# Kernel optimization log

Hardware: AMD Instinct MI355X
Metric: run time of the kernel (lower is better)

## Reference

```python
import jax, jax.numpy as jnp
import numpy as np

V, D, H, L, FF, T, B, W = 32000, 1024, 16, 8, 4096, 1024, 2, 256
HALF = FF // 2
HD = D // H
EPS = 1e-5


def layer_norm(x, g, b):
    mu = jnp.mean(x, axis=-1, keepdims=True)
    var = jnp.mean(jnp.square(x - mu), axis=-1, keepdims=True)
    return (x - mu) * jax.lax.rsqrt(var + EPS) * g + b


def setup_inputs() -> dict:
    key = jax.random.key(0)
    ks = jax.random.split(key, 12)
    s = 0.02
    nrm = lambda k, shape: jax.random.normal(k, shape, jnp.float32) * s
    idx = jax.random.randint(ks[0], (B, T), 0, V, dtype=jnp.int64)
    return {
        "idx": idx,
        "tok_emb": nrm(ks[1], (V, D)),
        "pos_emb": nrm(ks[2], (T, D)),
        "ln1_g": jnp.ones((L, D), jnp.float32),
        "ln1_b": jnp.zeros((L, D), jnp.float32),
        "qkv_w": nrm(ks[3], (L, 3 * D, D)),
        "out_w": nrm(ks[4], (L, D, D)),
        "ln2_g": jnp.ones((L, D), jnp.float32),
        "ln2_b": jnp.zeros((L, D), jnp.float32),
        "a_w1": nrm(ks[5], (L, HALF, D)),
        "a_w2": nrm(ks[6], (L, D, HALF)),
        "f_w1": nrm(ks[7], (L, HALF, D)),
        "f_w2": nrm(ks[8], (L, D, HALF)),
        "lnf_g": jnp.ones((D,), jnp.float32),
        "lnf_b": jnp.zeros((D,), jnp.float32),
        "head_w": nrm(ks[9], (V, D)),
    }


def _forward(idx, tok_emb, pos_emb, ln1_g, ln1_b, qkv_w, out_w, ln2_g, ln2_b,
             a_w1, a_w2, f_w1, f_w2, lnf_g, lnf_b, head_w):
    Bc, Tc = idx.shape
    x = tok_emb[idx] + pos_emb[:Tc]  # [B,T,D]
    # sliding-window causal band: attend to j in [i-W+1, i]
    i = jnp.arange(Tc)
    d = i[:, None] - i[None, :]
    mask = jnp.where((d >= 0) & (d < W), 0.0, -jnp.inf).astype(x.dtype)  # [T,T]
    scale = 1.0 / np.sqrt(HD)

    def block(x, p):
        l1g, l1b, qw, ow, l2g, l2b, aw1, aw2, fw1, fw2 = p
        h = layer_norm(x, l1g, l1b)
        qkv = (h @ qw.T).reshape(Bc, Tc, 3, H, HD)
        q, k, v = qkv[:, :, 0], qkv[:, :, 1], qkv[:, :, 2]  # [B,T,H,HD]
        attn = jnp.einsum('bqhd,bkhd->bhqk', q, k) * scale + mask
        attn = jax.nn.softmax(attn, axis=-1)
        o = jnp.einsum('bhqk,bkhd->bqhd', attn, v).reshape(Bc, Tc, D)
        x = x + o @ ow.T
        h2 = layer_norm(x, l2g, l2b)
        mlp = (jax.nn.gelu(h2 @ aw1.T, approximate=False) @ aw2.T
               + jax.nn.gelu(h2 @ fw1.T, approximate=False) @ fw2.T)
        return x + mlp, None

    x, _ = jax.lax.scan(block, x, (ln1_g, ln1_b, qkv_w, out_w, ln2_g, ln2_b,
                                   a_w1, a_w2, f_w1, f_w2))
    return layer_norm(x, lnf_g, lnf_b) @ head_w.T  # [B,T,V]


def reference(idx, tok_emb, pos_emb, ln1_g, ln1_b, qkv_w, out_w, ln2_g, ln2_b,
              a_w1, a_w2, f_w1, f_w2, lnf_g, lnf_b, head_w):
    return _forward(idx, tok_emb, pos_emb, ln1_g, ln1_b, qkv_w, out_w,
                    ln2_g, ln2_b, a_w1, a_w2, f_w1, f_w2, lnf_g, lnf_b, head_w)
```

## Files before the change

kernel.cpp:

```cpp
#include <hip/hip_runtime.h>

typedef __bf16 bf16x8 __attribute__((ext_vector_type(8)));
typedef __bf16 bf16x4 __attribute__((ext_vector_type(4)));
typedef float  f32x4  __attribute__((ext_vector_type(4)));
typedef unsigned int u32x4 __attribute__((ext_vector_type(4)));

#define MFMA16(a, b, c) __builtin_amdgcn_mfma_f32_16x16x32_bf16(a, b, c, 0, 0, 0)

__device__ __forceinline__ void gload_lds16(const void* g, void* l) {
  __builtin_amdgcn_global_load_lds(
      (const __attribute__((address_space(1))) void*)g,
      (__attribute__((address_space(3))) void*)l, 16, 0, 0);
}

__device__ __forceinline__ void waitvm(int vm) {
  if (vm == 6)      asm volatile("s_waitcnt vmcnt(6)" ::: "memory");
  else if (vm == 4) asm volatile("s_waitcnt vmcnt(4)" ::: "memory");
  else if (vm == 3) asm volatile("s_waitcnt vmcnt(3)" ::: "memory");
  else              asm volatile("s_waitcnt vmcnt(0)" ::: "memory");
}

__global__ __launch_bounds__(256) void cvt_kernel(
    const float* __restrict__ s, __bf16* __restrict__ d, int n8) {
  int i = blockIdx.x * 256 + threadIdx.x;
  if (i >= n8) return;
  size_t o = (size_t)i * 8;
  f32x4 a = *(const f32x4*)(s + o), b = *(const f32x4*)(s + o + 4);
  bf16x8 v;
  v[0] = (__bf16)a[0]; v[1] = (__bf16)a[1]; v[2] = (__bf16)a[2]; v[3] = (__bf16)a[3];
  v[4] = (__bf16)b[0]; v[5] = (__bf16)b[1]; v[6] = (__bf16)b[2]; v[7] = (__bf16)b[3];
  *(bf16x8*)(d + o) = v;
}

__global__ __launch_bounds__(256) void cat_w1_kernel(
    const float* __restrict__ a, const float* __restrict__ f, __bf16* __restrict__ d) {
  int i = blockIdx.x * 256 + threadIdx.x;
  int k = (i & 127) * 8;
  int r = i >> 7;
  const float* s = (r < 2048) ? a + ((size_t)r << 10) + k
                              : f + ((size_t)(r - 2048) << 10) + k;
  f32x4 va = *(const f32x4*)s, vb = *(const f32x4*)(s + 4);
  bf16x8 v;
  v[0] = (__bf16)va[0]; v[1] = (__bf16)va[1]; v[2] = (__bf16)va[2]; v[3] = (__bf16)va[3];
  v[4] = (__bf16)vb[0]; v[5] = (__bf16)vb[1]; v[6] = (__bf16)vb[2]; v[7] = (__bf16)vb[3];
  *(bf16x8*)(d + ((size_t)i << 3)) = v;
}

__global__ __launch_bounds__(256) void cat_w2_kernel(
    const float* __restrict__ a, const float* __restrict__ f, __bf16* __restrict__ d) {
  int i = blockIdx.x * 256 + threadIdx.x;
  int k = (i & 511) * 8;
  int r = i >> 9;
  const float* s = (k < 2048) ? a + (size_t)r * 2048 + k
                              : f + (size_t)r * 2048 + (k - 2048);
  f32x4 va = *(const f32x4*)s, vb = *(const f32x4*)(s + 4);
  bf16x8 v;
  v[0] = (__bf16)va[0]; v[1] = (__bf16)va[1]; v[2] = (__bf16)va[2]; v[3] = (__bf16)va[3];
  v[4] = (__bf16)vb[0]; v[5] = (__bf16)vb[1]; v[6] = (__bf16)vb[2]; v[7] = (__bf16)vb[3];
  *(bf16x8*)(d + ((size_t)i << 3)) = v;
}

__global__ __launch_bounds__(256) void embed_kernel(
    const int* __restrict__ idx, const float* __restrict__ te,
    const float* __restrict__ pe, float* __restrict__ x) {
  int m = blockIdx.x;
  int t = m & 1023;
  int tok = idx[m];
  int c = threadIdx.x * 4;
  f32x4 a = *(const f32x4*)(te + (size_t)tok * 1024 + c);
  f32x4 p = *(const f32x4*)(pe + (size_t)t * 1024 + c);
  *(f32x4*)(x + (size_t)m * 1024 + c) = a + p;
}

__global__ __launch_bounds__(256) void ln_kernel(
    const float* __restrict__ x, const float* __restrict__ g,
    const float* __restrict__ bb, __bf16* __restrict__ out) {
  int row = blockIdx.x, tid = threadIdx.x;
  int wid = tid >> 6, lane = tid & 63;
  f32x4 v = *(const f32x4*)(x + (size_t)row * 1024 + tid * 4);
  float s = v[0] + v[1] + v[2] + v[3];
  #pragma unroll
  for (int off = 32; off >= 1; off >>= 1) s += __shfl_xor(s, off);
  __shared__ float red1[4], red2[4];
  if (lane == 0) red1[wid] = s;
  __syncthreads();
  float mu = (red1[0] + red1[1] + red1[2] + red1[3]) * (1.0f / 1024.0f);
  float d0 = v[0] - mu, d1 = v[1] - mu, d2 = v[2] - mu, d3 = v[3] - mu;
  float q = d0 * d0 + d1 * d1 + d2 * d2 + d3 * d3;
  #pragma unroll
  for (int off = 32; off >= 1; off >>= 1) q += __shfl_xor(q, off);
  if (lane == 0) red2[wid] = q;
  __syncthreads();
  float var = (red2[0] + red2[1] + red2[2] + red2[3]) * (1.0f / 1024.0f);
  float inv = rsqrtf(var + 1e-5f);
  f32x4 gg = *(const f32x4*)(g + tid * 4);
  f32x4 bv = *(const f32x4*)(bb + tid * 4);
  bf16x4 o4;
  o4[0] = (__bf16)(d0 * inv * gg[0] + bv[0]);
  o4[1] = (__bf16)(d1 * inv * gg[1] + bv[1]);
  o4[2] = (__bf16)(d2 * inv * gg[2] + bv[2]);
  o4[3] = (__bf16)(d3 * inv * gg[3] + bv[3]);
  *(bf16x4*)(out + (size_t)row * 1024 + tid * 4) = o4;
}

template <int EPI>
__global__ __launch_bounds__(512, 2) void gemm256(
    const __bf16* __restrict__ A, int lda,
    const __bf16* __restrict__ B, int ldb, int K,
    float* __restrict__ Cf, __bf16* __restrict__ Cb, int ldc, int nbx) {
  __shared__ __align__(16) __bf16 lds[49152];
  const int tid = threadIdx.x, lane = tid & 63, w = tid >> 6;
  const int l15 = lane & 15, l4 = lane >> 4;
  const int wr = w >> 2, wc = w & 3;

  int nwg = gridDim.x, id = blockIdx.x;
  int q = nwg >> 3, r = nwg & 7;
  int xcd = id & 7, pos = id >> 3;
  int nid = (xcd < r ? xcd * (q + 1) : r * (q + 1) + (xcd - r) * q) + pos;
  int row0 = (nid % nbx) * 256, col0 = (nid / nbx) * 256;

  const __bf16* ag = A + (size_t)row0 * lda;
  const __bf16* bg = B + (size_t)col0 * ldb;

  f32x4 acc[8][4];
  #pragma unroll
  for (int i = 0; i < 8; ++i)
    #pragma unroll
    for (int j = 0; j < 4; ++j) acc[i][j] = (f32x4){0.f, 0.f, 0.f, 0.f};

  int srow[2], scol[2];
  #pragma unroll
  for (int i = 0; i < 2; ++i) {
    int p = (w + i * 8) * 1024 + lane * 16;
    int row = p >> 6, ch = (p >> 4) & 3;
    srow[i] = row;
    scol[i] = (ch ^ ((row >> 1) & 3)) * 8;
  }
  const int fx = (((l4 << 4) ^ (((l15 >> 1) & 3) << 4)) >> 1);

  auto stageA = [&](int t, int c) {
    #pragma unroll
    for (int i = 0; i < 2; ++i)
      gload_lds16(ag + (size_t)srow[i] * lda + t * 32 + scol[i],
                  &lds[c * 16384 + (w + i * 8) * 512]);
  };
  auto stageB = [&](int t, int c) {
    #pragma unroll
    for (int i = 0; i < 2; ++i)
      gload_lds16(bg + (size_t)srow[i] * ldb + t * 32 + scol[i],
                  &lds[c * 16384 + 8192 + (w + i * 8) * 512]);
  };

  auto kgroup = [&](int t2, int c, int cn, int vm, bool stg) {
    if (stg) stageA(t2, cn);
    waitvm(vm);
    __builtin_amdgcn_sched_barrier(0);
    __builtin_amdgcn_s_barrier();
    __builtin_amdgcn_sched_barrier(0);
    const int cb = c * 16384;
    bf16x8 bfr[4], af[4];
    #pragma unroll
    for (int ni = 0; ni < 4; ++ni)
      bfr[ni] = *(const bf16x8*)&lds[cb + 8192 + (wc * 64 + ni * 16 + l15) * 32 + fx];
    #pragma unroll
    for (int mi = 0; mi < 4; ++mi)
      af[mi] = *(const bf16x8*)&lds[cb + (wr * 128 + mi * 16 + l15) * 32 + fx];
    __builtin_amdgcn_s_setprio(1);
    #pragma unroll
    for (int mi = 0; mi < 4; ++mi)
      #pragma unroll
      for (int ni = 0; ni < 4; ++ni)
        acc[mi][ni] = MFMA16(af[mi], bfr[ni], acc[mi][ni]);
    __builtin_amdgcn_s_setprio(0);
    #pragma unroll
    for (int mi = 0; mi < 4; ++mi)
      af[mi] = *(const bf16x8*)&lds[cb + (wr * 128 + (mi + 4) * 16 + l15) * 32 + fx];
    if (stg) stageB(t2, cn);
    __builtin_amdgcn_s_setprio(1);
    #pragma unroll
    for (int mi = 0; mi < 4; ++mi)
      #pragma unroll
      for (int ni = 0; ni < 4; ++ni)
        acc[mi + 4][ni] = MFMA16(af[mi], bfr[ni], acc[mi + 4][ni]);
    __builtin_amdgcn_s_setprio(0);
    __builtin_amdgcn_sched_barrier(0);
    __builtin_amdgcn_s_barrier();
    __builtin_amdgcn_sched_barrier(0);
  };

  const int NT = K >> 5;
  stageA(0, 0); stageB(0, 0);
  stageA(1, 1); stageB(1, 1);

  int c = 0;
  for (int t = 0; t < NT - 2; ++t) {
    int cn = c + 2; if (cn >= 3) cn -= 3;
    kgroup(t + 2, c, cn, 6, true);
    c = (c == 2) ? 0 : c + 1;
  }
  kgroup(0, c, 0, 4, false);
  c = (c == 2) ? 0 : c + 1;
  kgroup(0, c, 0, 0, false);

  #pragma unroll
  for (int mi = 0; mi < 8; ++mi)
    #pragma unroll
    for (int ni = 0; ni < 4; ++ni)
      #pragma unroll
      for (int rr = 0; rr < 4; ++rr) {
        int row = row0 + wr * 128 + mi * 16 + l4 * 4 + rr;
        int col = col0 + wc * 64 + ni * 16 + l15;
        float v = acc[mi][ni][rr];
        size_t off = (size_t)row * ldc + col;
        if (EPI == 0) {
          Cf[off] = v;
        } else if (EPI == 1) {
          Cb[off] = (__bf16)v;
        } else {
          float gv = 0.5f * v * (1.0f + erff(v * 0.70710678118654752f));
          Cb[off] = (__bf16)gv;
        }
      }
}

template <int BN, int EPI>
__global__ __launch_bounds__(256) void gemm_bf16(
    const __bf16* __restrict__ A, int lda,
    const __bf16* __restrict__ B, int ldb, int K,
    float* __restrict__ Cf, __bf16* __restrict__ Cb, int ldc,
    const float* __restrict__ resid, int nbx) {
  constexpr int ACCN = BN / 32;
  constexpr int LB = BN / 64;
  constexpr int L = 2 + LB;
  __shared__ __align__(16) __bf16 As[2 * 4096];
  __shared__ __align__(16) __bf16 Bs[2 * BN * 32];

  int nwg = gridDim.x, id = blockIdx.x;
  int q = nwg >> 3, r = nwg & 7;
  int xcd = id & 7, pos = id >> 3;
  int nid = (xcd < r ? xcd * (q + 1) : r * (q + 1) + (xcd - r) * q) + pos;
  int row0 = (nid % nbx) * 128;
  int col0 = (nid / nbx) * BN;

  const int tid = threadIdx.x, lane = tid & 63, wid = tid >> 6;
  const int l15 = lane & 15, l4 = lane >> 4;
  const int wr = wid >> 1, wc = wid & 1;
  const int fx = (((l4 << 4) ^ (((l15 >> 1) & 3) << 4)) >> 1);

  f32x4 acc[4][ACCN];
  #pragma unroll
  for (int i = 0; i < 4; ++i)
    #pragma unroll
    for (int j = 0; j < ACCN; ++j) acc[i][j] = (f32x4){0.f, 0.f, 0.f, 0.f};

  const __bf16* aptr = A + (size_t)row0 * lda;
  const __bf16* bptr = B + (size_t)col0 * ldb;

  auto stage = [&](int t, int p) {
    #pragma unroll
    for (int i = 0; i < 2; ++i) {
      int ch = tid + 256 * i;
      int rr = ch >> 2, kc = ch & 3;
      gload_lds16(aptr + (size_t)rr * lda + t * 32 + (kc ^ ((rr >> 1) & 3)) * 8,
                  &As[p * 4096 + ch * 8]);
    }
    #pragma unroll
    for (int i = 0; i < LB; ++i) {
      int ch = tid + 256 * i;
      int rr = ch >> 2, kc = ch & 3;
      gload_lds16(bptr + (size_t)rr * ldb + t * 32 + (kc ^ ((rr >> 1) & 3)) * 8,
                  &Bs[p * BN * 32 + ch * 8]);
    }
  };

  const int NT = K >> 5;
  stage(0, 0);
  for (int t = 0; t < NT; ++t) {
    int p = t & 1;
    bool stg = (t + 1 < NT);
    if (stg) stage(t + 1, p ^ 1);
    waitvm(stg ? L : 0);
    __builtin_amdgcn_sched_barrier(0);
    __builtin_amdgcn_s_barrier();
    __builtin_amdgcn_sched_barrier(0);
    bf16x8 af[4], bfr[ACCN];
    #pragma unroll
    for (int mi = 0; mi < 4; ++mi)
      af[mi] = *(const bf16x8*)&As[p * 4096 + (wr * 64 + mi * 16 + l15) * 32 + fx];
    #pragma unroll
    for (int ni = 0; ni < ACCN; ++ni)
      bfr[ni] = *(const bf16x8*)&Bs[p * BN * 32 + (wc * (BN / 2) + ni * 16 + l15) * 32 + fx];
    #pragma unroll
    for (int mi = 0; mi < 4; ++mi)
      #pragma unroll
      for (int ni = 0; ni < ACCN; ++ni)
        acc[mi][ni] = MFMA16(af[mi], bfr[ni], acc[mi][ni]);
    __builtin_amdgcn_sched_barrier(0);
    __builtin_amdgcn_s_barrier();
    __builtin_amdgcn_sched_barrier(0);
  }

  #pragma unroll
  for (int mi = 0; mi < 4; ++mi)
    #pragma unroll
    for (int ni = 0; ni < ACCN; ++ni)
      #pragma unroll
      for (int rr = 0; rr < 4; ++rr) {
        int row = row0 + wr * 64 + mi * 16 + l4 * 4 + rr;
        int col = col0 + wc * (BN / 2) + ni * 16 + l15;
        float v = acc[mi][ni][rr];
        size_t off = (size_t)row * ldc + col;
        if (EPI == 0) {
          Cf[off] = v;
        } else if (EPI == 1) {
          Cb[off] = (__bf16)v;
        } else if (EPI == 2) {
          float gv = 0.5f * v * (1.0f + erff(v * 0.70710678118654752f));
          Cb[off] = (__bf16)gv;
        } else {
          Cf[off] = resid[off] + v;
        }
      }
}

__global__ __launch_bounds__(256) void attn_kernel(
    const __bf16* __restrict__ qkv, __bf16* __restrict__ o) {
  const int bid = blockIdx.x;
  const int qt = bid & 15, h = (bid >> 4) & 15, b = bid >> 8;
  const int qs = qt * 64;
  const int ntiles = (qt + 1 < 5) ? (qt + 1) : 5;
  const int kt0 = qt - (ntiles - 1);

  __shared__ __align__(16) __bf16 Qs[64][72];
  __shared__ __align__(16) __bf16 KVs[64][72];
  __shared__ __align__(16) __bf16 Ssm[64][328];
  __shared__ float rsum[64];

  const int tid = threadIdx.x;
  const int lane = tid & 63, wid = tid >> 6;
  const int l15 = lane & 15, l4 = lane >> 4;
  const size_t rs = 3072;
  const __bf16* qbase = qkv + ((size_t)(b * 1024 + qs)) * rs + h * 64;

  #pragma unroll
  for (int i = 0; i < 2; ++i) {
    int c = tid * 2 + i;
    int rr = c >> 3, dc = c & 7;
    *(u32x4*)&Qs[rr][dc * 8] = *(const u32x4*)(qbase + (size_t)rr * rs + dc * 8);
  }

  for (int it = 0; it < ntiles; ++it) {
    int kt = kt0 + it;
    const __bf16* kbase = qkv + ((size_t)(b * 1024 + kt * 64)) * rs + 1024 + h * 64;
    __syncthreads();
    #pragma unroll
    for (int i = 0; i < 2; ++i) {
      int c = tid * 2 + i;
      int rr = c >> 3, dc = c & 7;
      *(u32x4*)&KVs[rr][dc * 8] = *(const u32x4*)(kbase + (size_t)rr * rs + dc * 8);
    }
    __syncthreads();
    bf16x8 aq[2];
    #pragma unroll
    for (int kk = 0; kk < 2; ++kk)
      aq[kk] = *(const bf16x8*)&Qs[16 * wid + l15][kk * 32 + l4 * 8];
    #pragma unroll
    for (int n = 0; n < 4; ++n) {
      f32x4 c4 = (f32x4){0.f, 0.f, 0.f, 0.f};
      #pragma unroll
      for (int kk = 0; kk < 2; ++kk) {
        bf16x8 bk = *(const bf16x8*)&KVs[n * 16 + l15][kk * 32 + l4 * 8];
        c4 = MFMA16(aq[kk], bk, c4);
      }
      int kj = kt * 64 + n * 16 + l15;
      int colS = it * 64 + n * 16 + l15;
      #pragma unroll
      for (int rr = 0; rr < 4; ++rr) {
        int qi = qs + 16 * wid + l4 * 4 + rr;
        int d = qi - kj;
        float sv = c4[rr] * 0.125f;
        Ssm[16 * wid + l4 * 4 + rr][colS] =
            (d >= 0 && d < 256) ? (__bf16)sv : (__bf16)(-1e30f);
      }
    }
  }

  for (int rr = 0; rr < 16; ++rr) {
    int row = 16 * wid + rr;
    float vals[5];
    #pragma unroll
    for (int i = 0; i < 5; ++i) vals[i] = -3e38f;
    #pragma unroll
    for (int i = 0; i < 5; ++i)
      if (i < ntiles) vals[i] = (float)Ssm[row][lane + 64 * i];
    float m = vals[0];
    #pragma unroll
    for (int i = 1; i < 5; ++i) m = fmaxf(m, vals[i]);
    #pragma unroll
    for (int off = 32; off >= 1; off >>= 1) m = fmaxf(m, __shfl_xor(m, off));
    float s = 0.f;
    #pragma unroll
    for (int i = 0; i < 5; ++i)
      if (i < ntiles) {
        float p = __expf(vals[i] - m);
        s += p;
        Ssm[row][lane + 64 * i] = (__bf16)p;
      }
    #pragma unroll
    for (int off = 32; off >= 1; off >>= 1) s += __shfl_xor(s, off);
    if (lane == 0) rsum[row] = s;
  }

  f32x4 oacc[4];
  #pragma unroll
  for (int n = 0; n < 4; ++n) oacc[n] = (f32x4){0.f, 0.f, 0.f, 0.f};

  for (int it = 0; it < ntiles; ++it) {
    int kt = kt0 + it;
    const __bf16* vbase = qkv + ((size_t)(b * 1024 + kt * 64)) * rs + 2048 + h * 64;
    __syncthreads();
    if (tid < 64) {
      int k0 = (tid >> 3) * 8, d0 = (tid & 7) * 8;
      bf16x8 vr[8];
      #pragma unroll
      for (int rr = 0; rr < 8; ++rr)
        vr[rr] = *(const bf16x8*)(vbase + (size_t)(k0 + rr) * rs + d0);
      #pragma unroll
      for (int j = 0; j < 8; ++j) {
        bf16x8 w;
        #pragma unroll
        for (int rr = 0; rr < 8; ++rr) w[rr] = vr[rr][j];
        *(bf16x8*)&KVs[d0 + j][k0] = w;
      }
    }
    __syncthreads();
    #pragma unroll
    for (int kk = 0; kk < 2; ++kk) {
      bf16x8 ap = *(const bf16x8*)&Ssm[16 * wid + l15][it * 64 + kk * 32 + l4 * 8];
      #pragma unroll
      for (int n = 0; n < 4; ++n) {
        bf16x8 bv = *(const bf16x8*)&KVs[n * 16 + l15][kk * 32 + l4 * 8];
        oacc[n] = MFMA16(ap, bv, oacc[n]);
      }
    }
  }

  #pragma unroll
  for (int n = 0; n < 4; ++n)
    #pragma unroll
    for (int rr = 0; rr < 4; ++rr) {
      int qrow = 16 * wid + l4 * 4 + rr;
      float inv = 1.0f / rsum[qrow];
      size_t m = (size_t)(b * 1024 + qs + qrow);
      o[m * 1024 + h * 64 + n * 16 + l15] = (__bf16)(oacc[n][rr] * inv);
    }
}

extern "C" void kernel_launch(void* const* d_in, const int* in_sizes, int n_in,
                              void* d_out, int out_size, void* d_ws, size_t ws_size,
                              hipStream_t stream) {
  (void)in_sizes; (void)n_in; (void)out_size;
  const int*   idx     = (const int*)d_in[0];
  const float* tok_emb = (const float*)d_in[1];
  const float* pos_emb = (const float*)d_in[2];
  const float* ln1_g   = (const float*)d_in[3];
  const float* ln1_b   = (const float*)d_in[4];
  const float* qkv_w   = (const float*)d_in[5];
  const float* out_w   = (const float*)d_in[6];
  const float* ln2_g   = (const float*)d_in[7];
  const float* ln2_b   = (const float*)d_in[8];
  const float* a_w1    = (const float*)d_in[9];
  const float* a_w2    = (const float*)d_in[10];
  const float* f_w1    = (const float*)d_in[11];
  const float* f_w2    = (const float*)d_in[12];
  const float* lnf_g   = (const float*)d_in[13];
  const float* lnf_b   = (const float*)d_in[14];
  const float* head_w  = (const float*)d_in[15];
  float* out = (float*)d_out;

  char* ws = (char*)d_ws;
  float*  x    = (float*)(ws);
  __bf16* h    = (__bf16*)(ws + 8388608);
  __bf16* qkv  = (__bf16*)(ws + 12582912);
  __bf16* oatt = (__bf16*)(ws + 25165824);
  __bf16* gcat = (__bf16*)(ws + 29360128);

  const bool full = ws_size >= 313000000ull;

  __bf16 *wq, *wo, *w1c, *w2c, *wh;
  if (full) {
    wq  = (__bf16*)(ws + 46137344);
    wo  = (__bf16*)(ws + 96468992);
    w1c = (__bf16*)(ws + 113246208);
    w2c = (__bf16*)(ws + 180355072);
    wh  = (__bf16*)(ws + 247463936);
    cvt_kernel<<<12288, 256, 0, stream>>>(qkv_w, wq, 3145728);
    cvt_kernel<<<4096, 256, 0, stream>>>(out_w, wo, 1048576);
    for (int l = 0; l < 8; ++l) {
      cat_w1_kernel<<<2048, 256, 0, stream>>>(
          a_w1 + (size_t)l * 2048 * 1024, f_w1 + (size_t)l * 2048 * 1024,
          w1c + (size_t)l * 4096 * 1024);
      cat_w2_kernel<<<2048, 256, 0, stream>>>(
          a_w2 + (size_t)l * 1024 * 2048, f_w2 + (size_t)l * 1024 * 2048,
          w2c + (size_t)l * 1024 * 4096);
    }
    cvt_kernel<<<16000, 256, 0, stream>>>(head_w, wh, 4096000);
  } else {
    wq  = (__bf16*)(ws + 46137344);
    wo  = (__bf16*)(ws + 52428800);
    w1c = (__bf16*)(ws + 54525952);
    w2c = (__bf16*)(ws + 62914560);
    wh  = (__bf16*)(ws + 46137344);
  }

  embed_kernel<<<2048, 256, 0, stream>>>(idx, tok_emb, pos_emb, x);

  for (int l = 0; l < 8; ++l) {
    const __bf16 *wq_l, *wo_l, *w1_l, *w2_l;
    if (full) {
      wq_l = wq + (size_t)l * 3072 * 1024;
      wo_l = wo + (size_t)l * 1024 * 1024;
      w1_l = w1c + (size_t)l * 4096 * 1024;
      w2_l = w2c + (size_t)l * 1024 * 4096;
    } else {
      cvt_kernel<<<1536, 256, 0, stream>>>(qkv_w + (size_t)l * 3072 * 1024, wq, 393216);
      cvt_kernel<<<512, 256, 0, stream>>>(out_w + (size_t)l * 1024 * 1024, wo, 131072);
      cat_w1_kernel<<<2048, 256, 0, stream>>>(
          a_w1 + (size_t)l * 2048 * 1024, f_w1 + (size_t)l * 2048 * 1024, w1c);
      cat_w2_kernel<<<2048, 256, 0, stream>>>(
          a_w2 + (size_t)l * 1024 * 2048, f_w2 + (size_t)l * 1024 * 2048, w2c);
      wq_l = wq; wo_l = wo; w1_l = w1c; w2_l = w2c;
    }

    ln_kernel<<<2048, 256, 0, stream>>>(x, ln1_g + l * 1024, ln1_b + l * 1024, h);
    gemm256<1><<<8 * 12, 512, 0, stream>>>(
        h, 1024, wq_l, 1024, 1024, nullptr, qkv, 3072, 8);
    attn_kernel<<<512, 256, 0, stream>>>(qkv, oatt);
    gemm_bf16<64, 3><<<16 * 16, 256, 0, stream>>>(
        oatt, 1024, wo_l, 1024, 1024, x, nullptr, 1024, x, 16);
    ln_kernel<<<2048, 256, 0, stream>>>(x, ln2_g + l * 1024, ln2_b + l * 1024, h);
    gemm256<2><<<8 * 16, 512, 0, stream>>>(
        h, 1024, w1_l, 1024, 1024, nullptr, gcat, 4096, 8);
    gemm_bf16<64, 3><<<16 * 16, 256, 0, stream>>>(
        gcat, 4096, w2_l, 4096, 4096, x, nullptr, 1024, x, 16);
  }

  if (!full) {
    cvt_kernel<<<16000, 256, 0, stream>>>(head_w, wh, 4096000);
  }
  ln_kernel<<<2048, 256, 0, stream>>>(x, lnf_g, lnf_b, h);
  gemm256<0><<<8 * 125, 512, 0, stream>>>(
      h, 1024, wh, 1024, 1024, out, nullptr, 32000, 8);
}
```

Before: 2.082 ms.

## Deepen GEMM LDS pipelines, retile QKV/FFN1 GEMMs, parallelize V transpose

The 256x256 GEMM moves from a 3-stage to a 4-stage LDS ring, with more LDS and one block per CU. The 128-row GEMM moves from double to triple buffering and raises wave priority around its MFMA loop. The QKV and first FFN projections now use the 128xBN GEMM with more, smaller tiles instead of the 256x256 kernel, which increases parallelism but reduces data reuse. The attention V transpose is spread over all 256 threads with 4-wide pieces instead of 64 threads with 8-wide pieces.

```diff
diff --git a/kernel.cpp b/kernel.cpp
--- a/kernel.cpp
+++ b/kernel.cpp
@@ -14,7 +14,9 @@
 }
 
 __device__ __forceinline__ void waitvm(int vm) {
-  if (vm == 6)      asm volatile("s_waitcnt vmcnt(6)" ::: "memory");
+  if (vm == 10)     asm volatile("s_waitcnt vmcnt(10)" ::: "memory");
+  else if (vm == 8) asm volatile("s_waitcnt vmcnt(8)" ::: "memory");
+  else if (vm == 6) asm volatile("s_waitcnt vmcnt(6)" ::: "memory");
   else if (vm == 4) asm volatile("s_waitcnt vmcnt(4)" ::: "memory");
   else if (vm == 3) asm volatile("s_waitcnt vmcnt(3)" ::: "memory");
   else              asm volatile("s_waitcnt vmcnt(0)" ::: "memory");
@@ -104,11 +106,11 @@
 }
 
 template <int EPI>
-__global__ __launch_bounds__(512, 2) void gemm256(
+__global__ __launch_bounds__(512, 1) void gemm256(
     const __bf16* __restrict__ A, int lda,
     const __bf16* __restrict__ B, int ldb, int K,
     float* __restrict__ Cf, __bf16* __restrict__ Cb, int ldc, int nbx) {
-  __shared__ __align__(16) __bf16 lds[49152];
+  __shared__ __align__(16) __bf16 lds[65536];
   const int tid = threadIdx.x, lane = tid & 63, w = tid >> 6;
   const int l15 = lane & 15, l4 = lane >> 4;
   const int wr = w >> 2, wc = w & 3;
@@ -191,15 +193,16 @@
   const int NT = K >> 5;
   stageA(0, 0); stageB(0, 0);
   stageA(1, 1); stageB(1, 1);
+  stageA(2, 2); stageB(2, 2);
 
   int c = 0;
-  for (int t = 0; t < NT - 2; ++t) {
-    int cn = c + 2; if (cn >= 3) cn -= 3;
-    kgroup(t + 2, c, cn, 6, true);
-    c = (c == 2) ? 0 : c + 1;
-  }
-  kgroup(0, c, 0, 4, false);
-  c = (c == 2) ? 0 : c + 1;
+  for (int t = 0; t < NT - 3; ++t) {
+    int cn = c + 3; if (cn >= 4) cn -= 4;
+    kgroup(t + 3, c, cn, 10, true);
+    c = (c + 1) & 3;
+  }
+  kgroup(0, c, 0, 8, false); c = (c + 1) & 3;
+  kgroup(0, c, 0, 4, false); c = (c + 1) & 3;
   kgroup(0, c, 0, 0, false);
 
   #pragma unroll
@@ -232,8 +235,8 @@
   constexpr int ACCN = BN / 32;
   constexpr int LB = BN / 64;
   constexpr int L = 2 + LB;
-  __shared__ __align__(16) __bf16 As[2 * 4096];
-  __shared__ __align__(16) __bf16 Bs[2 * BN * 32];
+  __shared__ __align__(16) __bf16 As[3 * 4096];
+  __shared__ __align__(16) __bf16 Bs[3 * BN * 32];
 
   int nwg = gridDim.x, id = blockIdx.x;
   int q = nwg >> 3, r = nwg & 7;
@@ -275,11 +278,15 @@
 
   const int NT = K >> 5;
   stage(0, 0);
+  stage(1, 1);
+  int p = 0;
   for (int t = 0; t < NT; ++t) {
-    int p = t & 1;
-    bool stg = (t + 1 < NT);
-    if (stg) stage(t + 1, p ^ 1);
-    waitvm(stg ? L : 0);
+    bool stg = (t + 2 < NT);
+    if (stg) {
+      int ps = p + 2; if (ps >= 3) ps -= 3;
+      stage(t + 2, ps);
+    }
+    waitvm(stg ? 2 * L : ((t + 1 < NT) ? L : 0));
     __builtin_amdgcn_sched_barrier(0);
     __builtin_amdgcn_s_barrier();
     __builtin_amdgcn_sched_barrier(0);
@@ -290,14 +297,17 @@
     #pragma unroll
     for (int ni = 0; ni < ACCN; ++ni)
       bfr[ni] = *(const bf16x8*)&Bs[p * BN * 32 + (wc * (BN / 2) + ni * 16 + l15) * 32 + fx];
+    __builtin_amdgcn_s_setprio(1);
     #pragma unroll
     for (int mi = 0; mi < 4; ++mi)
       #pragma unroll
       for (int ni = 0; ni < ACCN; ++ni)
         acc[mi][ni] = MFMA16(af[mi], bfr[ni], acc[mi][ni]);
+    __builtin_amdgcn_s_setprio(0);
     __builtin_amdgcn_sched_barrier(0);
     __builtin_amdgcn_s_barrier();
     __builtin_amdgcn_sched_barrier(0);
+    p = (p == 2) ? 0 : p + 1;
   }
 
   #pragma unroll
@@ -402,9 +412,9 @@
     #pragma unroll
     for (int i = 0; i < 5; ++i)
       if (i < ntiles) {
-        float p = __expf(vals[i] - m);
-        s += p;
-        Ssm[row][lane + 64 * i] = (__bf16)p;
+        float pp = __expf(vals[i] - m);
+        s += pp;
+        Ssm[row][lane + 64 * i] = (__bf16)pp;
       }
     #pragma unroll
     for (int off = 32; off >= 1; off >>= 1) s += __shfl_xor(s, off);
@@ -419,18 +429,18 @@
     int kt = kt0 + it;
     const __bf16* vbase = qkv + ((size_t)(b * 1024 + kt * 64)) * rs + 2048 + h * 64;
     __syncthreads();
-    if (tid < 64) {
-      int k0 = (tid >> 3) * 8, d0 = (tid & 7) * 8;
-      bf16x8 vr[8];
-      #pragma unroll
-      for (int rr = 0; rr < 8; ++rr)
-        vr[rr] = *(const bf16x8*)(vbase + (size_t)(k0 + rr) * rs + d0);
-      #pragma unroll
-      for (int j = 0; j < 8; ++j) {
-        bf16x8 w;
+    {
+      int k0 = (tid >> 4) * 4, d0 = (tid & 15) * 4;
+      bf16x4 vr[4];
+      #pragma unroll
+      for (int rr = 0; rr < 4; ++rr)
+        vr[rr] = *(const bf16x4*)(vbase + (size_t)(k0 + rr) * rs + d0);
+      #pragma unroll
+      for (int j = 0; j < 4; ++j) {
+        bf16x4 wv;
         #pragma unroll
-        for (int rr = 0; rr < 8; ++rr) w[rr] = vr[rr][j];
-        *(bf16x8*)&KVs[d0 + j][k0] = w;
+        for (int rr = 0; rr < 4; ++rr) wv[rr] = vr[rr][j];
+        *(bf16x4*)&KVs[d0 + j][k0] = wv;
       }
     }
     __syncthreads();
@@ -533,14 +543,14 @@
     }
 
     ln_kernel<<<2048, 256, 0, stream>>>(x, ln1_g + l * 1024, ln1_b + l * 1024, h);
-    gemm256<1><<<8 * 12, 512, 0, stream>>>(
-        h, 1024, wq_l, 1024, 1024, nullptr, qkv, 3072, 8);
+    gemm_bf16<128, 1><<<16 * 24, 256, 0, stream>>>(
+        h, 1024, wq_l, 1024, 1024, nullptr, qkv, 3072, nullptr, 16);
     attn_kernel<<<512, 256, 0, stream>>>(qkv, oatt);
     gemm_bf16<64, 3><<<16 * 16, 256, 0, stream>>>(
         oatt, 1024, wo_l, 1024, 1024, x, nullptr, 1024, x, 16);
     ln_kernel<<<2048, 256, 0, stream>>>(x, ln2_g + l * 1024, ln2_b + l * 1024, h);
-    gemm256<2><<<8 * 16, 512, 0, stream>>>(
-        h, 1024, w1_l, 1024, 1024, nullptr, gcat, 4096, 8);
+    gemm_bf16<128, 2><<<16 * 32, 256, 0, stream>>>(
+        h, 1024, w1_l, 1024, 1024, nullptr, gcat, 4096, nullptr, 16);
     gemm_bf16<64, 3><<<16 * 16, 256, 0, stream>>>(
         gcat, 4096, w2_l, 4096, 4096, x, nullptr, 1024, x, 16);
   }
```

Result: faster. 1.983 ms (-4.8%).
